# Performance work log

Hardware: AMD Instinct MI355X
Metric: run time of the kernel (lower is better)

## Reference

```python
import jax, jax.numpy as jnp
import numpy as np

DIM = 384
NUM_HEADS = 6
HEAD_DIM = DIM // NUM_HEADS
SCALE = HEAD_DIM ** -0.5


def setup_inputs() -> dict:
    key = jax.random.key(0)
    k_x, k_qkvw, k_qkvb, k_pw, k_pb = jax.random.split(key, 5)
    B, N, C = 8, 2048, DIM
    x = jax.random.normal(k_x, (B, N, C), dtype=jnp.float32)
    # nn.Linear weights stored as (out, in); apply as x @ W.T + b
    s = 1.0 / np.sqrt(C)
    qkv_w = jax.random.uniform(k_qkvw, (3 * C, C), minval=-s, maxval=s, dtype=jnp.float32)
    qkv_b = jax.random.uniform(k_qkvb, (3 * C,), minval=-s, maxval=s, dtype=jnp.float32)
    proj_w = jax.random.uniform(k_pw, (C, C), minval=-s, maxval=s, dtype=jnp.float32)
    proj_b = jax.random.uniform(k_pb, (C,), minval=-s, maxval=s, dtype=jnp.float32)
    return {"x": x, "qkv_w": qkv_w, "qkv_b": qkv_b, "proj_w": proj_w,
            "proj_b": proj_b, "h": 64, "w": 32}


def reference(x, qkv_w, qkv_b, proj_w, proj_b, h, w):
    B, N, C = x.shape
    H, D = NUM_HEADS, HEAD_DIM
    qkv = x @ qkv_w.T + qkv_b              # [B, N, 3C]
    qkv = qkv.reshape(B, N, 3, H, D)
    q = qkv[:, :, 0].transpose(0, 2, 1, 3) * SCALE  # [B, H, N, D]
    k = qkv[:, :, 1].transpose(0, 2, 1, 3)
    v = qkv[:, :, 2].transpose(0, 2, 1, 3)
    attn = jnp.einsum('bhnd,bhmd->bhnm', q, k)      # [B, H, N, N]
    attn = jax.nn.softmax(attn, axis=-1)
    out = jnp.einsum('bhnm,bhmd->bhnd', attn, v)    # [B, H, N, D]
    out = out.transpose(0, 2, 1, 3).reshape(B, N, C)
    return out @ proj_w.T + proj_b
```

## Files before the change

### kernel.cpp

```cpp
#include <hip/hip_runtime.h>

typedef __attribute__((ext_vector_type(8))) short bf16x8;
typedef __attribute__((ext_vector_type(4))) float f32x4;
typedef __attribute__((ext_vector_type(16))) float f32x16;
typedef __attribute__((ext_vector_type(4))) unsigned int u32x4;

#define DIMC 384
#define NHEADS 6
#define HDIM 64
#define BATCH 8
#define SEQ 2048
#define TOKENS (BATCH*SEQ)
#define QKV_OUT (3*DIMC)

__device__ __forceinline__ unsigned short f2bf(float f) {
  unsigned int u = __float_as_uint(f);
  u += 0x7fffu + ((u >> 16) & 1u);
  return (unsigned short)(u >> 16);
}

__device__ __forceinline__ unsigned int cvt_pk_bf16(float a, float b) {
  unsigned int r;
  asm volatile("v_cvt_pk_bf16_f32 %0, %1, %2" : "=v"(r) : "v"(a), "v"(b));
  return r;
}

__device__ __forceinline__ void async_load16(const void* g, void* l) {
  __builtin_amdgcn_global_load_lds(
      (const __attribute__((address_space(1))) unsigned int*)g,
      (__attribute__((address_space(3))) unsigned int*)l, 16, 0, 0);
}

#define N4_X   (TOKENS*DIMC/4)
#define N4_W1  (QKV_OUT*DIMC/4)
#define N4_W2  (DIMC*DIMC/4)
__global__ void cast3_kernel(const float* __restrict__ x,
                             const float* __restrict__ w1,
                             const float* __restrict__ w2,
                             unsigned short* __restrict__ ox,
                             unsigned short* __restrict__ o1,
                             unsigned short* __restrict__ o2) {
  int i = blockIdx.x * blockDim.x + threadIdx.x;
  const int stride = gridDim.x * blockDim.x;
  for (; i < N4_X + N4_W1 + N4_W2; i += stride) {
    const float* src; unsigned short* dst; int j = i;
    if (j < N4_X)            { src = x;  dst = ox; }
    else if (j < N4_X+N4_W1) { j -= N4_X; src = w1; dst = o1; }
    else                     { j -= N4_X+N4_W1; src = w2; dst = o2; }
    float4 v = ((const float4*)src)[j];
    ushort4 o;
    o.x = f2bf(v.x); o.y = f2bf(v.y); o.z = f2bf(v.z); o.w = f2bf(v.w);
    ((ushort4*)dst)[j] = o;
  }
}

__global__ __launch_bounds__(256) void qkv_gemm_kernel(
    const unsigned short* __restrict__ A,
    const unsigned short* __restrict__ W,
    const float* __restrict__ bias,
    unsigned short* __restrict__ Qb,
    unsigned short* __restrict__ Kb,
    unsigned short* __restrict__ Vtb) {
  __shared__ unsigned short As[3][128*32];
  __shared__ unsigned short Bs[3][128*32];
  const int tid = threadIdx.x;
  const int w = tid >> 6, l = tid & 63;
  const int wm = w >> 1, wn = w & 1;
  const int q4 = l >> 4, r15 = l & 15;
  const int wg = blockIdx.x;
  const int logical = (wg & 7) * 144 + (wg >> 3);
  const int row = logical / 9, col = logical % 9;
  const int m0 = row * 128;
  const int n0 = col * 128;

  f32x4 acc[4][4];
#pragma unroll
  for (int i = 0; i < 4; i++)
#pragma unroll
    for (int j = 0; j < 4; j++) acc[i][j] = f32x4{0.f, 0.f, 0.f, 0.f};

  const int arow = l >> 2;
  const int achk = l & 3;
  const unsigned short* Asrc = A + (size_t)(m0 + w*16 + arow) * 384 + achk * 8;
  const unsigned short* Wsrc = W + (size_t)(n0 + w*16 + arow) * 384 + achk * 8;

#pragma unroll
  for (int cc = 0; cc < 2; ++cc) {
    async_load16(Asrc + cc*64*384, (char*)&As[0][0] + cc*4096 + w*1024);
    async_load16(Wsrc + cc*64*384, (char*)&Bs[0][0] + cc*4096 + w*1024);
  }

  int cur = 0;
  for (int kt = 0; kt < 12; ++kt) {
    const int nxt = (cur == 2) ? 0 : cur + 1;
    if (kt < 11) {
#pragma unroll
      for (int cc = 0; cc < 2; ++cc) {
        async_load16(Asrc + (kt+1)*32 + cc*64*384, (char*)&As[0][0] + nxt*8192 + cc*4096 + w*1024);
        async_load16(Wsrc + (kt+1)*32 + cc*64*384, (char*)&Bs[0][0] + nxt*8192 + cc*4096 + w*1024);
      }
      asm volatile("s_waitcnt vmcnt(4)" ::: "memory");
    } else {
      asm volatile("s_waitcnt vmcnt(0)" ::: "memory");
    }
    __builtin_amdgcn_s_barrier();
    asm volatile("" ::: "memory");
    const unsigned short* asb = &As[0][0] + cur*4096;
    const unsigned short* bsb = &Bs[0][0] + cur*4096;
    bf16x8 a[4], b[4];
#pragma unroll
    for (int mi = 0; mi < 4; mi++)
      a[mi] = *(const bf16x8*)(asb + (wm*64 + mi*16 + r15)*32 + q4*8);
#pragma unroll
    for (int ni = 0; ni < 4; ni++)
      b[ni] = *(const bf16x8*)(bsb + (wn*64 + ni*16 + r15)*32 + q4*8);
    __builtin_amdgcn_s_setprio(1);
#pragma unroll
    for (int mi = 0; mi < 4; mi++)
#pragma unroll
      for (int ni = 0; ni < 4; ni++)
        acc[mi][ni] = __builtin_amdgcn_mfma_f32_16x16x32_bf16(
            a[mi], b[ni], acc[mi][ni], 0, 0, 0);
    __builtin_amdgcn_s_setprio(0);
    cur = nxt;
  }
  const int c3 = col / 3;
  const int nrel0 = (col % 3) * 128 + wn * 64;
  if (c3 == 2) {
#pragma unroll
    for (int ni = 0; ni < 4; ni++) {
      int ncol = nrel0 + ni*16 + r15;
      float bv = bias[n0 + wn*64 + ni*16 + r15];
      int h = ncol >> 6, d = ncol & 63;
#pragma unroll
      for (int mi = 0; mi < 4; mi++) {
        int m = m0 + wm*64 + mi*16 + 4*q4;
        int bb = m >> 11, t = m & 2047;
        ushort4 pk;
        pk.x = f2bf(acc[mi][ni][0] + bv);
        pk.y = f2bf(acc[mi][ni][1] + bv);
        pk.z = f2bf(acc[mi][ni][2] + bv);
        pk.w = f2bf(acc[mi][ni][3] + bv);
        *(ushort4*)(Vtb + ((size_t)(bb*NHEADS + h)*HDIM + d)*SEQ + t) = pk;
      }
    }
  } else {
    unsigned short* D = (c3 == 0) ? Qb : Kb;
    const float scale = (c3 == 0) ? 0.125f * 1.4426950408889634f : 1.0f;
#pragma unroll
    for (int ni = 0; ni < 4; ni++) {
      int ncol = nrel0 + ni*16 + r15;
      float bv = bias[n0 + wn*64 + ni*16 + r15];
      int h = ncol >> 6, d = ncol & 63;
#pragma unroll
      for (int mi = 0; mi < 4; mi++) {
#pragma unroll
        for (int reg = 0; reg < 4; reg++) {
          int m = m0 + wm*64 + mi*16 + 4*q4 + reg;
          int bb = m >> 11, t = m & 2047;
          float v = (acc[mi][ni][reg] + bv) * scale;
          D[((size_t)(bb*NHEADS + h)*SEQ + t)*HDIM + d] = f2bf(v);
        }
      }
    }
  }
}

__global__ __launch_bounds__(256, 3) void flash_kernel(
    const unsigned short* __restrict__ Q, const unsigned short* __restrict__ K,
    const unsigned short* __restrict__ Vt, unsigned short* __restrict__ O2) {
  __shared__ unsigned short Ks[3][64*64];
  __shared__ unsigned short Vs[3][64*64];
  const int tid = threadIdx.x;
  const int w = tid >> 6, l = tid & 63;
  const int hl = l >> 5, l31 = l & 31, l7 = l & 7;
  const int wg = blockIdx.x;
  const int logical = (wg & 7) * 96 + (wg >> 3);
  const int qt = logical & 15, bh = logical >> 4;
  const unsigned short* Qp = Q  + (size_t)bh * SEQ * HDIM;
  const unsigned short* Kp = K  + (size_t)bh * SEQ * HDIM;
  const unsigned short* Vp = Vt + (size_t)bh * HDIM * SEQ;

  const int qrow = qt*128 + w*32 + l31;
  bf16x8 qf[4];
#pragma unroll
  for (int ks = 0; ks < 4; ks++)
    qf[ks] = *(const bf16x8*)(Qp + (size_t)qrow*HDIM + ks*16 + hl*8);

  const int srow = w*8 + (l >> 3);
  const int sch  = l7 ^ (l >> 3) ^ w;
  const unsigned short* Ksrc = Kp + (size_t)srow*HDIM + sch*8;
  const unsigned short* Vsrc = Vp + (size_t)srow*SEQ  + sch*8;

  const int swl = (l31 >> 3) & 3;
  int rdoff[4];
#pragma unroll
  for (int ks = 0; ks < 4; ks++)
    rdoff[ks] = l31*128 + (((ks*2 + hl) ^ l7 ^ swl) << 4);

  f32x16 o0 = {}, o1 = {};
  float l_run = 0.f;

  async_load16(Ksrc,           (char*)&Ks[0][0] + w*1024);
  async_load16(Ksrc + 32*HDIM, (char*)&Ks[0][0] + w*1024 + 4096);
  async_load16(Vsrc,           (char*)&Vs[0][0] + w*1024);
  async_load16(Vsrc + 32*SEQ,  (char*)&Vs[0][0] + w*1024 + 4096);

  int cur = 0;
  for (int kt = 0; kt < 32; ++kt) {
    const int nxt = (cur == 2) ? 0 : cur + 1;
    if (kt < 31) {
      const unsigned short* ks_ = Ksrc + (size_t)(kt+1)*64*HDIM;
      const unsigned short* vs_ = Vsrc + (size_t)(kt+1)*64;
      char* kd = (char*)&Ks[0][0] + nxt*8192 + w*1024;
      char* vd = (char*)&Vs[0][0] + nxt*8192 + w*1024;
      async_load16(ks_,           kd);
      async_load16(ks_ + 32*HDIM, kd + 4096);
      async_load16(vs_,           vd);
      async_load16(vs_ + 32*SEQ,  vd + 4096);
      asm volatile("s_waitcnt vmcnt(4)" ::: "memory");
    } else {
      asm volatile("s_waitcnt vmcnt(0)" ::: "memory");
    }
    __builtin_amdgcn_s_barrier();
    asm volatile("" ::: "memory");

    const char* ksb = (const char*)&Ks[0][0] + cur*8192;
    const char* vsb = (const char*)&Vs[0][0] + cur*8192;

    bf16x8 pa0, pa1;
    float lsumA;
    {
      f32x16 s = {};
      __builtin_amdgcn_s_setprio(1);
#pragma unroll
      for (int ks = 0; ks < 4; ks++) {
        bf16x8 kf = *(const bf16x8*)(ksb + rdoff[ks]);
        s = __builtin_amdgcn_mfma_f32_32x32x16_bf16(kf, qf[ks], s, 0, 0, 0);
      }
      __builtin_amdgcn_s_setprio(0);
      unsigned int Y[4][2];
      float lsum = 0.f;
#pragma unroll
      for (int h = 0; h < 4; h++) {
        float a0 = __builtin_amdgcn_exp2f(s[4*h+0]);
        float a1 = __builtin_amdgcn_exp2f(s[4*h+1]);
        float a2 = __builtin_amdgcn_exp2f(s[4*h+2]);
        float a3 = __builtin_amdgcn_exp2f(s[4*h+3]);
        lsum += (a0+a1)+(a2+a3);
        Y[h][0] = cvt_pk_bf16(a0, a1);
        Y[h][1] = cvt_pk_bf16(a2, a3);
      }
      lsumA = lsum;
      {
        unsigned int x0 = Y[0][0], x1 = Y[0][1], y0 = Y[1][0], y1 = Y[1][1];
        asm volatile("v_permlane32_swap_b32 %0, %1" : "+v"(x0), "+v"(y0));
        asm volatile("v_permlane32_swap_b32 %0, %1" : "+v"(x1), "+v"(y1));
        u32x4 t; t[0] = x0; t[1] = x1; t[2] = y0; t[3] = y1;
        union { u32x4 u; bf16x8 b; } cvt; cvt.u = t;
        pa0 = cvt.b;
      }
      {
        unsigned int x0 = Y[2][0], x1 = Y[2][1], y0 = Y[3][0], y1 = Y[3][1];
        asm volatile("v_permlane32_swap_b32 %0, %1" : "+v"(x0), "+v"(y0));
        asm volatile("v_permlane32_swap_b32 %0, %1" : "+v"(x1), "+v"(y1));
        u32x4 t; t[0] = x0; t[1] = x1; t[2] = y0; t[3] = y1;
        union { u32x4 u; bf16x8 b; } cvt; cvt.u = t;
        pa1 = cvt.b;
      }
    }
    __builtin_amdgcn_sched_barrier(0);

    bf16x8 pa2, pa3;
    float lsumB;
    {
      f32x16 s = {};
      __builtin_amdgcn_s_setprio(1);
#pragma unroll
      for (int ks = 0; ks < 4; ks++) {
        bf16x8 kf = *(const bf16x8*)(ksb + 4096 + rdoff[ks]);
        s = __builtin_amdgcn_mfma_f32_32x32x16_bf16(kf, qf[ks], s, 0, 0, 0);
      }
      __builtin_amdgcn_s_setprio(0);
      unsigned int Y[4][2];
      float lsum = 0.f;
#pragma unroll
      for (int h = 0; h < 4; h++) {
        float a0 = __builtin_amdgcn_exp2f(s[4*h+0]);
        float a1 = __builtin_amdgcn_exp2f(s[4*h+1]);
        float a2 = __builtin_amdgcn_exp2f(s[4*h+2]);
        float a3 = __builtin_amdgcn_exp2f(s[4*h+3]);
        lsum += (a0+a1)+(a2+a3);
        Y[h][0] = cvt_pk_bf16(a0, a1);
        Y[h][1] = cvt_pk_bf16(a2, a3);
      }
      lsumB = lsum;
      {
        unsigned int x0 = Y[0][0], x1 = Y[0][1], y0 = Y[1][0], y1 = Y[1][1];
        asm volatile("v_permlane32_swap_b32 %0, %1" : "+v"(x0), "+v"(y0));
        asm volatile("v_permlane32_swap_b32 %0, %1" : "+v"(x1), "+v"(y1));
        u32x4 t; t[0] = x0; t[1] = x1; t[2] = y0; t[3] = y1;
        union { u32x4 u; bf16x8 b; } cvt; cvt.u = t;
        pa2 = cvt.b;
      }
      {
        unsigned int x0 = Y[2][0], x1 = Y[2][1], y0 = Y[3][0], y1 = Y[3][1];
        asm volatile("v_permlane32_swap_b32 %0, %1" : "+v"(x0), "+v"(y0));
        asm volatile("v_permlane32_swap_b32 %0, %1" : "+v"(x1), "+v"(y1));
        u32x4 t; t[0] = x0; t[1] = x1; t[2] = y0; t[3] = y1;
        union { u32x4 u; bf16x8 b; } cvt; cvt.u = t;
        pa3 = cvt.b;
      }
    }
    l_run += lsumA + lsumB;
    __builtin_amdgcn_sched_barrier(0);

    __builtin_amdgcn_s_setprio(1);
    {
      bf16x8 vf0 = *(const bf16x8*)(vsb + rdoff[0]);
      bf16x8 vf1 = *(const bf16x8*)(vsb + 4096 + rdoff[0]);
      o0 = __builtin_amdgcn_mfma_f32_32x32x16_bf16(pa0, vf0, o0, 0, 0, 0);
      o1 = __builtin_amdgcn_mfma_f32_32x32x16_bf16(pa0, vf1, o1, 0, 0, 0);
      vf0 = *(const bf16x8*)(vsb + rdoff[1]);
      vf1 = *(const bf16x8*)(vsb + 4096 + rdoff[1]);
      o0 = __builtin_amdgcn_mfma_f32_32x32x16_bf16(pa1, vf0, o0, 0, 0, 0);
      o1 = __builtin_amdgcn_mfma_f32_32x32x16_bf16(pa1, vf1, o1, 0, 0, 0);
      vf0 = *(const bf16x8*)(vsb + rdoff[2]);
      vf1 = *(const bf16x8*)(vsb + 4096 + rdoff[2]);
      o0 = __builtin_amdgcn_mfma_f32_32x32x16_bf16(pa2, vf0, o0, 0, 0, 0);
      o1 = __builtin_amdgcn_mfma_f32_32x32x16_bf16(pa2, vf1, o1, 0, 0, 0);
      vf0 = *(const bf16x8*)(vsb + rdoff[3]);
      vf1 = *(const bf16x8*)(vsb + 4096 + rdoff[3]);
      o0 = __builtin_amdgcn_mfma_f32_32x32x16_bf16(pa3, vf0, o0, 0, 0, 0);
      o1 = __builtin_amdgcn_mfma_f32_32x32x16_bf16(pa3, vf1, o1, 0, 0, 0);
    }
    __builtin_amdgcn_s_setprio(0);
    cur = nxt;
  }

  l_run += __shfl_xor(l_run, 32, 64);
  const float linv = 1.0f / l_run;
  const int b = bh / NHEADS, h = bh % NHEADS;
#pragma unroll
  for (int reg = 0; reg < 16; reg++) {
    const int qr = (reg & 3) + 8*(reg >> 2) + 4*hl;
    const float lr = __shfl(linv, qr, 64);
    const int t = qt*128 + w*32 + qr;
    unsigned short* dst = O2 + ((size_t)(b*SEQ + t))*DIMC + h*HDIM;
    dst[l31]      = f2bf(o0[reg] * lr);
    dst[32 + l31] = f2bf(o1[reg] * lr);
  }
}

__global__ __launch_bounds__(256) void proj_gemm_kernel(
    const unsigned short* __restrict__ A,
    const unsigned short* __restrict__ W,
    const float* __restrict__ bias,
    float* __restrict__ out) {
  __shared__ unsigned short As[3][128*32];
  __shared__ unsigned short Bs[3][64*32];
  const int tid = threadIdx.x;
  const int w = tid >> 6, l = tid & 63;
  const int q4 = l >> 4, r15 = l & 15;
  const int wg = blockIdx.x;
  const int logical = (wg & 7) * 96 + (wg >> 3);
  const int row = logical / 6, col = logical % 6;
  const int m0 = row * 128;
  const int n0 = col * 64;

  f32x4 acc[2][4];
#pragma unroll
  for (int i = 0; i < 2; i++)
#pragma unroll
    for (int j = 0; j < 4; j++) acc[i][j] = f32x4{0.f, 0.f, 0.f, 0.f};

  const int arow = l >> 2;
  const int achk = l & 3;
  const unsigned short* Asrc = A + (size_t)(m0 + w*16 + arow) * 384 + achk * 8;
  const unsigned short* Wsrc = W + (size_t)(n0 + w*16 + arow) * 384 + achk * 8;

#pragma unroll
  for (int cc = 0; cc < 2; ++cc)
    async_load16(Asrc + cc*64*384, (char*)&As[0][0] + cc*4096 + w*1024);
  async_load16(Wsrc, (char*)&Bs[0][0] + w*1024);

  int cur = 0;
  for (int kt = 0; kt < 12; ++kt) {
    const int nxt = (cur == 2) ? 0 : cur + 1;
    if (kt < 11) {
#pragma unroll
      for (int cc = 0; cc < 2; ++cc)
        async_load16(Asrc + (kt+1)*32 + cc*64*384,
                     (char*)&As[0][0] + nxt*8192 + cc*4096 + w*1024);
      async_load16(Wsrc + (kt+1)*32, (char*)&Bs[0][0] + nxt*4096 + w*1024);
      asm volatile("s_waitcnt vmcnt(3)" ::: "memory");
    } else {
      asm volatile("s_waitcnt vmcnt(0)" ::: "memory");
    }
    __builtin_amdgcn_s_barrier();
    asm volatile("" ::: "memory");
    const unsigned short* asb = &As[0][0] + cur*4096;
    const unsigned short* bsb = &Bs[0][0] + cur*2048;
    bf16x8 a[2], b[4];
#pragma unroll
    for (int mi = 0; mi < 2; mi++)
      a[mi] = *(const bf16x8*)(asb + (w*32 + mi*16 + r15)*32 + q4*8);
#pragma unroll
    for (int ni = 0; ni < 4; ni++)
      b[ni] = *(const bf16x8*)(bsb + (ni*16 + r15)*32 + q4*8);
    __builtin_amdgcn_s_setprio(1);
#pragma unroll
    for (int mi = 0; mi < 2; mi++)
#pragma unroll
      for (int ni = 0; ni < 4; ni++)
        acc[mi][ni] = __builtin_amdgcn_mfma_f32_16x16x32_bf16(
            a[mi], b[ni], acc[mi][ni], 0, 0, 0);
    __builtin_amdgcn_s_setprio(0);
    cur = nxt;
  }
#pragma unroll
  for (int ni = 0; ni < 4; ni++) {
    int ncol = n0 + ni*16 + r15;
    float bv = bias[ncol];
#pragma unroll
    for (int mi = 0; mi < 2; mi++) {
#pragma unroll
      for (int reg = 0; reg < 4; reg++) {
        int m = m0 + w*32 + mi*16 + 4*q4 + reg;
        out[(size_t)m * DIMC + ncol] = acc[mi][ni][reg] + bv;
      }
    }
  }
}

extern "C" void kernel_launch(void* const* d_in, const int* in_sizes, int n_in,
                              void* d_out, int out_size, void* d_ws, size_t ws_size,
                              hipStream_t stream) {
  const float* x      = (const float*)d_in[0];
  const float* qkv_w  = (const float*)d_in[1];
  const float* qkv_b  = (const float*)d_in[2];
  const float* proj_w = (const float*)d_in[3];
  const float* proj_b = (const float*)d_in[4];
  float* out = (float*)d_out;

  unsigned short* xbf   = (unsigned short*)d_ws;
  unsigned short* wqkv  = xbf   + (size_t)TOKENS * DIMC;
  unsigned short* wproj = wqkv  + (size_t)QKV_OUT * DIMC;
  unsigned short* Qb    = wproj + (size_t)DIMC * DIMC;
  unsigned short* Kb    = Qb    + (size_t)TOKENS * DIMC;
  unsigned short* Vtb   = Kb    + (size_t)TOKENS * DIMC;
  unsigned short* A2    = Vtb   + (size_t)TOKENS * DIMC;

  cast3_kernel<<<2048, 256, 0, stream>>>(x, qkv_w, proj_w, xbf, wqkv, wproj);
  qkv_gemm_kernel<<<1152, 256, 0, stream>>>(xbf, wqkv, qkv_b, Qb, Kb, Vtb);
  flash_kernel<<<768, 256, 0, stream>>>(Qb, Kb, Vtb, A2);
  proj_gemm_kernel<<<768, 256, 0, stream>>>(A2, wproj, proj_b, out);
}
```

Measured before the change: 114.7 us.

## Give each flash wave two 32-row query tiles with 128-thread blocks

The flash kernel now runs 2 waves per block instead of 4, and each wave handles 64 query rows as two 32-row sub-tiles. Each K and V fragment read from LDS therefore feeds twice as many MFMAs, cutting LDS read traffic per unit of compute. Each wave now issues 8 async loads per tile to stage the shared K/V tiles, and the softmax code is moved into a macro. In exchange, register pressure roughly doubles (four output accumulators, eight P fragments), which may reduce occupancy or cause spills. There are also fewer waves per block to hide latency.

```diff
diff --git a/kernel.cpp b/kernel.cpp
--- a/kernel.cpp
+++ b/kernel.cpp
@@ -166,7 +166,39 @@
   }
 }
 
-__global__ __launch_bounds__(256, 3) void flash_kernel(
+#define SOFTMAX_PACK(S, PLO, PHI, LACC) do {                                 \
+    unsigned int Y[4][2];                                                    \
+    float lsum = 0.f;                                                        \
+    _Pragma("unroll")                                                        \
+    for (int h = 0; h < 4; h++) {                                            \
+      float a0 = __builtin_amdgcn_exp2f(S[4*h+0]);                           \
+      float a1 = __builtin_amdgcn_exp2f(S[4*h+1]);                           \
+      float a2 = __builtin_amdgcn_exp2f(S[4*h+2]);                           \
+      float a3 = __builtin_amdgcn_exp2f(S[4*h+3]);                           \
+      lsum += (a0+a1)+(a2+a3);                                               \
+      Y[h][0] = cvt_pk_bf16(a0, a1);                                         \
+      Y[h][1] = cvt_pk_bf16(a2, a3);                                         \
+    }                                                                        \
+    LACC += lsum;                                                            \
+    {                                                                        \
+      unsigned int x0 = Y[0][0], x1 = Y[0][1], y0 = Y[1][0], y1 = Y[1][1];   \
+      asm volatile("v_permlane32_swap_b32 %0, %1" : "+v"(x0), "+v"(y0));     \
+      asm volatile("v_permlane32_swap_b32 %0, %1" : "+v"(x1), "+v"(y1));     \
+      u32x4 t; t[0] = x0; t[1] = x1; t[2] = y0; t[3] = y1;                   \
+      union { u32x4 u; bf16x8 b; } cvt; cvt.u = t;                           \
+      PLO = cvt.b;                                                           \
+    }                                                                        \
+    {                                                                        \
+      unsigned int x0 = Y[2][0], x1 = Y[2][1], y0 = Y[3][0], y1 = Y[3][1];   \
+      asm volatile("v_permlane32_swap_b32 %0, %1" : "+v"(x0), "+v"(y0));     \
+      asm volatile("v_permlane32_swap_b32 %0, %1" : "+v"(x1), "+v"(y1));     \
+      u32x4 t; t[0] = x0; t[1] = x1; t[2] = y0; t[3] = y1;                   \
+      union { u32x4 u; bf16x8 b; } cvt; cvt.u = t;                           \
+      PHI = cvt.b;                                                           \
+    }                                                                        \
+  } while (0)
+
+__global__ __launch_bounds__(128, 2) void flash_kernel(
     const unsigned short* __restrict__ Q, const unsigned short* __restrict__ K,
     const unsigned short* __restrict__ Vt, unsigned short* __restrict__ O2) {
   __shared__ unsigned short Ks[3][64*64];
@@ -181,16 +213,24 @@
   const unsigned short* Kp = K  + (size_t)bh * SEQ * HDIM;
   const unsigned short* Vp = Vt + (size_t)bh * HDIM * SEQ;
 
-  const int qrow = qt*128 + w*32 + l31;
-  bf16x8 qf[4];
-#pragma unroll
-  for (int ks = 0; ks < 4; ks++)
-    qf[ks] = *(const bf16x8*)(Qp + (size_t)qrow*HDIM + ks*16 + hl*8);
-
-  const int srow = w*8 + (l >> 3);
-  const int sch  = l7 ^ (l >> 3) ^ w;
-  const unsigned short* Ksrc = Kp + (size_t)srow*HDIM + sch*8;
-  const unsigned short* Vsrc = Vp + (size_t)srow*SEQ  + sch*8;
+  const int q0 = qt*128 + w*64;
+  bf16x8 qf0[4], qf1[4];
+#pragma unroll
+  for (int ks = 0; ks < 4; ks++) {
+    qf0[ks] = *(const bf16x8*)(Qp + (size_t)(q0 + l31)*HDIM      + ks*16 + hl*8);
+    qf1[ks] = *(const bf16x8*)(Qp + (size_t)(q0 + 32 + l31)*HDIM + ks*16 + hl*8);
+  }
+
+  const int r3 = l >> 3;
+  const unsigned short* KsrcJ[4];
+  const unsigned short* VsrcJ[4];
+#pragma unroll
+  for (int j = 0; j < 4; j++) {
+    const int srow = w*32 + j*8 + r3;
+    const int sch  = l7 ^ r3 ^ j;
+    KsrcJ[j] = Kp + (size_t)srow*HDIM + sch*8;
+    VsrcJ[j] = Vp + (size_t)srow*SEQ  + sch*8;
+  }
 
   const int swl = (l31 >> 3) & 3;
   int rdoff[4];
@@ -198,27 +238,27 @@
   for (int ks = 0; ks < 4; ks++)
     rdoff[ks] = l31*128 + (((ks*2 + hl) ^ l7 ^ swl) << 4);
 
-  f32x16 o0 = {}, o1 = {};
-  float l_run = 0.f;
-
-  async_load16(Ksrc,           (char*)&Ks[0][0] + w*1024);
-  async_load16(Ksrc + 32*HDIM, (char*)&Ks[0][0] + w*1024 + 4096);
-  async_load16(Vsrc,           (char*)&Vs[0][0] + w*1024);
-  async_load16(Vsrc + 32*SEQ,  (char*)&Vs[0][0] + w*1024 + 4096);
+  f32x16 o00 = {}, o01 = {}, o10 = {}, o11 = {};
+  float l_run0 = 0.f, l_run1 = 0.f;
+
+#pragma unroll
+  for (int j = 0; j < 4; j++) {
+    async_load16(KsrcJ[j], (char*)&Ks[0][0] + w*4096 + j*1024);
+    async_load16(VsrcJ[j], (char*)&Vs[0][0] + w*4096 + j*1024);
+  }
 
   int cur = 0;
   for (int kt = 0; kt < 32; ++kt) {
     const int nxt = (cur == 2) ? 0 : cur + 1;
     if (kt < 31) {
-      const unsigned short* ks_ = Ksrc + (size_t)(kt+1)*64*HDIM;
-      const unsigned short* vs_ = Vsrc + (size_t)(kt+1)*64;
-      char* kd = (char*)&Ks[0][0] + nxt*8192 + w*1024;
-      char* vd = (char*)&Vs[0][0] + nxt*8192 + w*1024;
-      async_load16(ks_,           kd);
-      async_load16(ks_ + 32*HDIM, kd + 4096);
-      async_load16(vs_,           vd);
-      async_load16(vs_ + 32*SEQ,  vd + 4096);
-      asm volatile("s_waitcnt vmcnt(4)" ::: "memory");
+      char* kd = (char*)&Ks[0][0] + nxt*8192 + w*4096;
+      char* vd = (char*)&Vs[0][0] + nxt*8192 + w*4096;
+#pragma unroll
+      for (int j = 0; j < 4; j++) {
+        async_load16(KsrcJ[j] + (size_t)(kt+1)*64*HDIM, kd + j*1024);
+        async_load16(VsrcJ[j] + (size_t)(kt+1)*64,      vd + j*1024);
+      }
+      asm volatile("s_waitcnt vmcnt(8)" ::: "memory");
     } else {
       asm volatile("s_waitcnt vmcnt(0)" ::: "memory");
     }
@@ -228,127 +268,92 @@
     const char* ksb = (const char*)&Ks[0][0] + cur*8192;
     const char* vsb = (const char*)&Vs[0][0] + cur*8192;
 
-    bf16x8 pa0, pa1;
-    float lsumA;
+    bf16x8 paA00, paA01, paA10, paA11;
     {
-      f32x16 s = {};
+      f32x16 s0 = {}, s1 = {};
       __builtin_amdgcn_s_setprio(1);
 #pragma unroll
       for (int ks = 0; ks < 4; ks++) {
         bf16x8 kf = *(const bf16x8*)(ksb + rdoff[ks]);
-        s = __builtin_amdgcn_mfma_f32_32x32x16_bf16(kf, qf[ks], s, 0, 0, 0);
+        s0 = __builtin_amdgcn_mfma_f32_32x32x16_bf16(kf, qf0[ks], s0, 0, 0, 0);
+        s1 = __builtin_amdgcn_mfma_f32_32x32x16_bf16(kf, qf1[ks], s1, 0, 0, 0);
       }
       __builtin_amdgcn_s_setprio(0);
-      unsigned int Y[4][2];
-      float lsum = 0.f;
-#pragma unroll
-      for (int h = 0; h < 4; h++) {
-        float a0 = __builtin_amdgcn_exp2f(s[4*h+0]);
-        float a1 = __builtin_amdgcn_exp2f(s[4*h+1]);
-        float a2 = __builtin_amdgcn_exp2f(s[4*h+2]);
-        float a3 = __builtin_amdgcn_exp2f(s[4*h+3]);
-        lsum += (a0+a1)+(a2+a3);
-        Y[h][0] = cvt_pk_bf16(a0, a1);
-        Y[h][1] = cvt_pk_bf16(a2, a3);
-      }
-      lsumA = lsum;
-      {
-        unsigned int x0 = Y[0][0], x1 = Y[0][1], y0 = Y[1][0], y1 = Y[1][1];
-        asm volatile("v_permlane32_swap_b32 %0, %1" : "+v"(x0), "+v"(y0));
-        asm volatile("v_permlane32_swap_b32 %0, %1" : "+v"(x1), "+v"(y1));
-        u32x4 t; t[0] = x0; t[1] = x1; t[2] = y0; t[3] = y1;
-        union { u32x4 u; bf16x8 b; } cvt; cvt.u = t;
-        pa0 = cvt.b;
-      }
-      {
-        unsigned int x0 = Y[2][0], x1 = Y[2][1], y0 = Y[3][0], y1 = Y[3][1];
-        asm volatile("v_permlane32_swap_b32 %0, %1" : "+v"(x0), "+v"(y0));
-        asm volatile("v_permlane32_swap_b32 %0, %1" : "+v"(x1), "+v"(y1));
-        u32x4 t; t[0] = x0; t[1] = x1; t[2] = y0; t[3] = y1;
-        union { u32x4 u; bf16x8 b; } cvt; cvt.u = t;
-        pa1 = cvt.b;
-      }
+      SOFTMAX_PACK(s0, paA00, paA01, l_run0);
+      SOFTMAX_PACK(s1, paA10, paA11, l_run1);
     }
     __builtin_amdgcn_sched_barrier(0);
 
-    bf16x8 pa2, pa3;
-    float lsumB;
+    bf16x8 paB00, paB01, paB10, paB11;
     {
-      f32x16 s = {};
+      f32x16 s0 = {}, s1 = {};
       __builtin_amdgcn_s_setprio(1);
 #pragma unroll
       for (int ks = 0; ks < 4; ks++) {
         bf16x8 kf = *(const bf16x8*)(ksb + 4096 + rdoff[ks]);
-        s = __builtin_amdgcn_mfma_f32_32x32x16_bf16(kf, qf[ks], s, 0, 0, 0);
+        s0 = __builtin_amdgcn_mfma_f32_32x32x16_bf16(kf, qf0[ks], s0, 0, 0, 0);
+        s1 = __builtin_amdgcn_mfma_f32_32x32x16_bf16(kf, qf1[ks], s1, 0, 0, 0);
       }
       __builtin_amdgcn_s_setprio(0);
-      unsigned int Y[4][2];
-      float lsum = 0.f;
-#pragma unroll
-      for (int h = 0; h < 4; h++) {
-        float a0 = __builtin_amdgcn_exp2f(s[4*h+0]);
-        float a1 = __builtin_amdgcn_exp2f(s[4*h+1]);
-        float a2 = __builtin_amdgcn_exp2f(s[4*h+2]);
-        float a3 = __builtin_amdgcn_exp2f(s[4*h+3]);
-        lsum += (a0+a1)+(a2+a3);
-        Y[h][0] = cvt_pk_bf16(a0, a1);
-        Y[h][1] = cvt_pk_bf16(a2, a3);
-      }
-      lsumB = lsum;
-      {
-        unsigned int x0 = Y[0][0], x1 = Y[0][1], y0 = Y[1][0], y1 = Y[1][1];
-        asm volatile("v_permlane32_swap_b32 %0, %1" : "+v"(x0), "+v"(y0));
-        asm volatile("v_permlane32_swap_b32 %0, %1" : "+v"(x1), "+v"(y1));
-        u32x4 t; t[0] = x0; t[1] = x1; t[2] = y0; t[3] = y1;
-        union { u32x4 u; bf16x8 b; } cvt; cvt.u = t;
-        pa2 = cvt.b;
-      }
-      {
-        unsigned int x0 = Y[2][0], x1 = Y[2][1], y0 = Y[3][0], y1 = Y[3][1];
-        asm volatile("v_permlane32_swap_b32 %0, %1" : "+v"(x0), "+v"(y0));
-        asm volatile("v_permlane32_swap_b32 %0, %1" : "+v"(x1), "+v"(y1));
-        u32x4 t; t[0] = x0; t[1] = x1; t[2] = y0; t[3] = y1;
-        union { u32x4 u; bf16x8 b; } cvt; cvt.u = t;
-        pa3 = cvt.b;
-      }
-    }
-    l_run += lsumA + lsumB;
+      SOFTMAX_PACK(s0, paB00, paB01, l_run0);
+      SOFTMAX_PACK(s1, paB10, paB11, l_run1);
+    }
     __builtin_amdgcn_sched_barrier(0);
 
     __builtin_amdgcn_s_setprio(1);
     {
-      bf16x8 vf0 = *(const bf16x8*)(vsb + rdoff[0]);
-      bf16x8 vf1 = *(const bf16x8*)(vsb + 4096 + rdoff[0]);
-      o0 = __builtin_amdgcn_mfma_f32_32x32x16_bf16(pa0, vf0, o0, 0, 0, 0);
-      o1 = __builtin_amdgcn_mfma_f32_32x32x16_bf16(pa0, vf1, o1, 0, 0, 0);
+      bf16x8 vf0, vf1;
+      vf0 = *(const bf16x8*)(vsb + rdoff[0]);
+      vf1 = *(const bf16x8*)(vsb + 4096 + rdoff[0]);
+      o00 = __builtin_amdgcn_mfma_f32_32x32x16_bf16(paA00, vf0, o00, 0, 0, 0);
+      o01 = __builtin_amdgcn_mfma_f32_32x32x16_bf16(paA00, vf1, o01, 0, 0, 0);
+      o10 = __builtin_amdgcn_mfma_f32_32x32x16_bf16(paA10, vf0, o10, 0, 0, 0);
+      o11 = __builtin_amdgcn_mfma_f32_32x32x16_bf16(paA10, vf1, o11, 0, 0, 0);
       vf0 = *(const bf16x8*)(vsb + rdoff[1]);
       vf1 = *(const bf16x8*)(vsb + 4096 + rdoff[1]);
-      o0 = __builtin_amdgcn_mfma_f32_32x32x16_bf16(pa1, vf0, o0, 0, 0, 0);
-      o1 = __builtin_amdgcn_mfma_f32_32x32x16_bf16(pa1, vf1, o1, 0, 0, 0);
+      o00 = __builtin_amdgcn_mfma_f32_32x32x16_bf16(paA01, vf0, o00, 0, 0, 0);
+      o01 = __builtin_amdgcn_mfma_f32_32x32x16_bf16(paA01, vf1, o01, 0, 0, 0);
+      o10 = __builtin_amdgcn_mfma_f32_32x32x16_bf16(paA11, vf0, o10, 0, 0, 0);
+      o11 = __builtin_amdgcn_mfma_f32_32x32x16_bf16(paA11, vf1, o11, 0, 0, 0);
       vf0 = *(const bf16x8*)(vsb + rdoff[2]);
       vf1 = *(const bf16x8*)(vsb + 4096 + rdoff[2]);
-      o0 = __builtin_amdgcn_mfma_f32_32x32x16_bf16(pa2, vf0, o0, 0, 0, 0);
-      o1 = __builtin_amdgcn_mfma_f32_32x32x16_bf16(pa2, vf1, o1, 0, 0, 0);
+      o00 = __builtin_amdgcn_mfma_f32_32x32x16_bf16(paB00, vf0, o00, 0, 0, 0);
+      o01 = __builtin_amdgcn_mfma_f32_32x32x16_bf16(paB00, vf1, o01, 0, 0, 0);
+      o10 = __builtin_amdgcn_mfma_f32_32x32x16_bf16(paB10, vf0, o10, 0, 0, 0);
+      o11 = __builtin_amdgcn_mfma_f32_32x32x16_bf16(paB10, vf1, o11, 0, 0, 0);
       vf0 = *(const bf16x8*)(vsb + rdoff[3]);
       vf1 = *(const bf16x8*)(vsb + 4096 + rdoff[3]);
-      o0 = __builtin_amdgcn_mfma_f32_32x32x16_bf16(pa3, vf0, o0, 0, 0, 0);
-      o1 = __builtin_amdgcn_mfma_f32_32x32x16_bf16(pa3, vf1, o1, 0, 0, 0);
+      o00 = __builtin_amdgcn_mfma_f32_32x32x16_bf16(paB01, vf0, o00, 0, 0, 0);
+      o01 = __builtin_amdgcn_mfma_f32_32x32x16_bf16(paB01, vf1, o01, 0, 0, 0);
+      o10 = __builtin_amdgcn_mfma_f32_32x32x16_bf16(paB11, vf0, o10, 0, 0, 0);
+      o11 = __builtin_amdgcn_mfma_f32_32x32x16_bf16(paB11, vf1, o11, 0, 0, 0);
     }
     __builtin_amdgcn_s_setprio(0);
     cur = nxt;
   }
 
-  l_run += __shfl_xor(l_run, 32, 64);
-  const float linv = 1.0f / l_run;
+  l_run0 += __shfl_xor(l_run0, 32, 64);
+  l_run1 += __shfl_xor(l_run1, 32, 64);
+  const float linv0 = 1.0f / l_run0;
+  const float linv1 = 1.0f / l_run1;
   const int b = bh / NHEADS, h = bh % NHEADS;
 #pragma unroll
   for (int reg = 0; reg < 16; reg++) {
     const int qr = (reg & 3) + 8*(reg >> 2) + 4*hl;
-    const float lr = __shfl(linv, qr, 64);
-    const int t = qt*128 + w*32 + qr;
-    unsigned short* dst = O2 + ((size_t)(b*SEQ + t))*DIMC + h*HDIM;
-    dst[l31]      = f2bf(o0[reg] * lr);
-    dst[32 + l31] = f2bf(o1[reg] * lr);
+    {
+      const float lr = __shfl(linv0, qr, 64);
+      const int t = q0 + qr;
+      unsigned short* dst = O2 + ((size_t)(b*SEQ + t))*DIMC + h*HDIM;
+      dst[l31]      = f2bf(o00[reg] * lr);
+      dst[32 + l31] = f2bf(o01[reg] * lr);
+    }
+    {
+      const float lr = __shfl(linv1, qr, 64);
+      const int t = q0 + 32 + qr;
+      unsigned short* dst = O2 + ((size_t)(b*SEQ + t))*DIMC + h*HDIM;
+      dst[l31]      = f2bf(o10[reg] * lr);
+      dst[32 + l31] = f2bf(o11[reg] * lr);
+    }
   }
 }
 
@@ -453,6 +458,6 @@
 
   cast3_kernel<<<2048, 256, 0, stream>>>(x, qkv_w, proj_w, xbf, wqkv, wproj);
   qkv_gemm_kernel<<<1152, 256, 0, stream>>>(xbf, wqkv, qkv_b, Qb, Kb, Vtb);
-  flash_kernel<<<768, 256, 0, stream>>>(Qb, Kb, Vtb, A2);
+  flash_kernel<<<768, 128, 0, stream>>>(Qb, Kb, Vtb, A2);
   proj_gemm_kernel<<<768, 256, 0, stream>>>(A2, wproj, proj_b, out);
 }
```

Measured after the change: 123.9 us. +8.1%, slower.
